# Performance work log

Measured on AMD Instinct MI355X. Metric: run time of the kernel, lower is better.

## Reference

```python
import jax, jax.numpy as jnp
import numpy as np

NV, NH, T, B = 4096, 1024, 64, 32
CDK = 2


def _bern(key, p):
    # torch.bernoulli: sample is non-differentiable
    return jax.lax.stop_gradient((jax.random.uniform(key, p.shape, p.dtype) < p).astype(p.dtype))


def setup_inputs() -> dict:
    key = jax.random.key(0)
    k1, k2, k3 = jax.random.split(key, 3)
    # binary spike-train style visible data [NV, T, B]
    v = (jax.random.uniform(k1, (NV, T, B)) < 0.5).astype(jnp.float32)
    W = 0.01 * jax.random.normal(k2, (NH, NV), jnp.float32)
    U = 0.01 * jax.random.normal(k3, (NH, NH), jnp.float32)
    return {
        "v": v,
        "W": W,
        "U": U,
        "b_v": jnp.zeros((NV,), jnp.float32),
        "b_h": jnp.zeros((NH,), jnp.float32),
        "b_init": jnp.zeros((NH,), jnp.float32),
        "CDk": CDK,
    }


def _cd_step(W, b_v, v_t, hid_bias, key, CDk):
    # hid_bias: [NH,B] = U @ r_lag + b_h[:,None] (or b_init[:,None] at t=0)
    keys = jax.random.split(key, 2 * CDk)
    r_data = jax.nn.sigmoid(W @ v_t + hid_bias)  # hidden means [NH,B]
    h = _bern(keys[0], r_data)
    for k in range(CDk - 1):  # CD-k Gibbs chain (fixed small unroll)
        vm = _bern(keys[2 * k + 1], jax.nn.sigmoid(W.T @ h + b_v[:, None]))
        h = _bern(keys[2 * k + 2], jax.nn.sigmoid(W @ vm + hid_bias))
    v_model = _bern(keys[2 * CDk - 1], jax.nn.sigmoid(W.T @ h + b_v[:, None]))
    return v_model, h, r_data


def reference(v, W, U, b_v, b_h, b_init, CDk):
    Tn = v.shape[1]
    key = jax.random.key(42)
    k0, ks = jax.random.split(key)
    # t = 0 uses b_init instead of U @ r_lag + b_h
    vm0, h0, r0 = _cd_step(W, b_v, v[:, 0, :], b_init[:, None], k0, CDk)
    keys = jax.random.split(ks, Tn - 1)
    v_rest = jnp.moveaxis(v[:, 1:, :], 1, 0)  # [T-1, NV, B]

    def step(r_lag, inp):
        v_t, kt = inp
        vm, h, r = _cd_step(W, b_v, v_t, U @ r_lag + b_h[:, None], kt, CDk)
        return r, (vm, h, r)  # recurrence carries hidden means r_data

    _, (vms, hs, rs) = jax.lax.scan(step, r0, (v_rest, keys))
    v_model = jnp.concatenate([vm0[:, None, :], jnp.moveaxis(vms, 0, 1)], axis=1)  # [NV,T,B]
    r_model = jnp.concatenate([h0[:, None, :], jnp.moveaxis(hs, 0, 1)], axis=1)    # [NH,T,B]
    rt = jnp.concatenate([r0[:, None, :], jnp.moveaxis(rs, 0, 1)], axis=1)         # [NH,T,B]
    return v_model, r_model, rt
```

## Files before the change

### kernel.cpp

```cpp
#include <hip/hip_runtime.h>
#include <cstdint>
#include <cstddef>
#include <math.h>


#define NVV 4096
#define NHH 1024
#define TT  64
#define BB  32
#define CC  2048

typedef int v4i  __attribute__((ext_vector_type(4)));
typedef int v16i __attribute__((ext_vector_type(16)));

__constant__ double SC6[6] = {0x1p-48, 0x1p-40, 0x1p-32, 0x1p-24, 0x1p-16, 0x1p-8};

__host__ __device__ __forceinline__ void tf2x32(uint32_t k0, uint32_t k1,
                                                uint32_t x0, uint32_t x1,
                                                uint32_t& o0, uint32_t& o1) {
  uint32_t ks2 = k0 ^ k1 ^ 0x1BD11BDAu;
#define TF_RND(r) { x0 += x1; x1 = (x1 << (r)) | (x1 >> (32 - (r))); x1 ^= x0; }
  x0 += k0; x1 += k1;
  TF_RND(13) TF_RND(15) TF_RND(26) TF_RND(6)
  x0 += k1;  x1 += ks2 + 1u;
  TF_RND(17) TF_RND(29) TF_RND(16) TF_RND(24)
  x0 += ks2; x1 += k0 + 2u;
  TF_RND(13) TF_RND(15) TF_RND(26) TF_RND(6)
  x0 += k0;  x1 += k1 + 3u;
  TF_RND(17) TF_RND(29) TF_RND(16) TF_RND(24)
  x0 += k1;  x1 += ks2 + 4u;
  TF_RND(13) TF_RND(15) TF_RND(26) TF_RND(6)
  x0 += ks2; x1 += k0 + 5u;
#undef TF_RND
  o0 = x0; o1 = x1;
}

__device__ __forceinline__ float tf_uniform(uint32_t k0, uint32_t k1, uint32_t j) {
  uint32_t o0, o1;
  tf2x32(k0, k1, 0u, j, o0, o1);
  uint32_t bits = o0 ^ o1;
  return __uint_as_float((bits >> 9) | 0x3f800000u) - 1.0f;
}

__device__ __forceinline__ void bern_sample(double logit, uint32_t k0, uint32_t k1,
                                            uint32_t j, float& p32, float& bit) {
  double pd = 1.0 / (1.0 + exp(-logit));
  p32 = (float)pd;
  float u = tf_uniform(k0, k1, j);
  bit = (u < p32) ? 1.0f : 0.0f;
}

__device__ __forceinline__ void step_key(int t, int phase,
                                         uint32_t rk00, uint32_t rk01,
                                         uint32_t rk10, uint32_t rk11,
                                         uint32_t& c0, uint32_t& c1) {
  uint32_t kt0, kt1;
  tf2x32(rk10, rk11, 0u, (uint32_t)(t > 0 ? t - 1 : 0), kt0, kt1);
  if (t == 0) { kt0 = rk00; kt1 = rk01; }
  tf2x32(kt0, kt1, 0u, (uint32_t)phase, c0, c1);
}

__device__ __forceinline__ void slice6(float w, signed char sb[6]) {
  long long v = __double2ll_rn((double)w * 0x1p48);
#pragma unroll
  for (int s = 0; s < 6; s++) {
    signed char b = (signed char)(v & 0xFF);
    sb[s] = b;
    v = (v - b) >> 8;
  }
}

__global__ __launch_bounds__(256)
void prepW(const float* __restrict__ W, signed char* __restrict__ Ws,
           signed char* __restrict__ WsT) {
  __shared__ float tl[64][65];
  int bi = blockIdx.x >> 6;
  int bj = blockIdx.x & 63;
  int n0 = bi * 64, k0 = bj * 64;
  int tid = threadIdx.x;
#pragma unroll
  for (int it = 0; it < 4; it++) {
    int r = (tid >> 4) + it * 16, c4 = (tid & 15) * 4;
    float4 q = *(const float4*)(W + (size_t)(n0 + r) * NVV + k0 + c4);
    tl[r][c4] = q.x; tl[r][c4 + 1] = q.y; tl[r][c4 + 2] = q.z; tl[r][c4 + 3] = q.w;
  }
  __syncthreads();
#pragma unroll
  for (int it = 0; it < 4; it++) {
    int r = (tid >> 4) + it * 16, c4 = (tid & 15) * 4;
    unsigned int pk[6] = {0, 0, 0, 0, 0, 0};
    for (int j = 0; j < 4; j++) {
      signed char sb[6]; slice6(tl[r][c4 + j], sb);
      for (int s = 0; s < 6; s++) pk[s] |= ((unsigned)(unsigned char)sb[s]) << (8 * j);
    }
    for (int s = 0; s < 6; s++)
      *(unsigned int*)(Ws + (size_t)s * NHH * NVV + (size_t)(n0 + r) * NVV + k0 + c4) = pk[s];
  }
#pragma unroll
  for (int it = 0; it < 4; it++) {
    int r = (tid >> 4) + it * 16, c4 = (tid & 15) * 4;
    unsigned int pk[6] = {0, 0, 0, 0, 0, 0};
    for (int j = 0; j < 4; j++) {
      signed char sb[6]; slice6(tl[c4 + j][r], sb);
      for (int s = 0; s < 6; s++) pk[s] |= ((unsigned)(unsigned char)sb[s]) << (8 * j);
    }
    for (int s = 0; s < 6; s++)
      *(unsigned int*)(WsT + (size_t)s * NVV * NHH + (size_t)(k0 + r) * NHH + n0 + c4) = pk[s];
  }
}

__global__ __launch_bounds__(256)
void prepVT(const float* __restrict__ v, signed char* __restrict__ vT) {
  __shared__ float tl[64][65];
  int bi = blockIdx.x >> 5;
  int bj = blockIdx.x & 31;
  int i0 = bi * 64, c0 = bj * 64;
  int tid = threadIdx.x;
#pragma unroll
  for (int it = 0; it < 4; it++) {
    int r = (tid >> 4) + it * 16, c4 = (tid & 15) * 4;
    float4 q = *(const float4*)(v + (size_t)(i0 + r) * CC + c0 + c4);
    tl[r][c4] = q.x; tl[r][c4 + 1] = q.y; tl[r][c4 + 2] = q.z; tl[r][c4 + 3] = q.w;
  }
  __syncthreads();
#pragma unroll
  for (int it = 0; it < 4; it++) {
    int cc = (tid >> 4) + it * 16, i4 = (tid & 15) * 4;
    unsigned int pk = 0;
    for (int j = 0; j < 4; j++)
      pk |= ((unsigned)(tl[i4 + j][cc] != 0.0f ? 1 : 0)) << (8 * j);
    *(unsigned int*)(vT + (size_t)(c0 + cc) * NVV + i0 + i4) = pk;
  }
}

__global__ __launch_bounds__(256)
void s0k(const signed char* __restrict__ vT, const signed char* __restrict__ Ws,
         double* __restrict__ WvT) {
  int wave = threadIdx.x >> 6, lane = threadIdx.x & 63;
  int lrow = lane & 31, lhalf = lane >> 5;
  int xcd = blockIdx.x & 7, idx = blockIdx.x >> 3;
  int bn = xcd * 2 + (idx >> 4);
  int bm = idx & 15;
  int m0 = bm * 128 + (wave & 1) * 64;
  int n0 = bn * 64 + (wave >> 1) * 32;

  v16i acc[2][6];
  for (int mt = 0; mt < 2; mt++)
    for (int s = 0; s < 6; s++)
      for (int e = 0; e < 16; e++) acc[mt][s][e] = 0;

  const signed char* a0 = vT + (size_t)(m0 + lrow) * NVV + 16 * lhalf;
  const signed char* a1 = a0 + (size_t)32 * NVV;
  const signed char* bB = Ws + (size_t)(n0 + lrow) * NVV + 16 * lhalf;
#pragma unroll 2
  for (int kb = 0; kb < NVV; kb += 32) {
    v4i af0 = *(const v4i*)(a0 + kb);
    v4i af1 = *(const v4i*)(a1 + kb);
#pragma unroll
    for (int s = 0; s < 6; s++) {
      v4i bf = *(const v4i*)(bB + (size_t)s * NHH * NVV + kb);
      acc[0][s] = __builtin_amdgcn_mfma_i32_32x32x32_i8(af0, bf, acc[0][s], 0, 0, 0);
      acc[1][s] = __builtin_amdgcn_mfma_i32_32x32x32_i8(af1, bf, acc[1][s], 0, 0, 0);
    }
  }
#pragma unroll
  for (int mt = 0; mt < 2; mt++)
#pragma unroll
    for (int e = 0; e < 16; e++) {
      int row = (e & 3) + 8 * (e >> 2) + 4 * lhalf;
      double lg = 0;
#pragma unroll
      for (int s = 0; s < 6; s++) lg += (double)acc[mt][s][e] * SC6[s];
      WvT[(size_t)(m0 + mt * 32 + row) * NHH + n0 + lrow] = lg;
    }
}

__global__ __launch_bounds__(256)
void step1(const float* __restrict__ U, const float* __restrict__ rin,
           float* __restrict__ rout, const double* __restrict__ WvT,
           const float* __restrict__ b_h, const float* __restrict__ b_init,
           float* __restrict__ rt, unsigned char* __restrict__ hT,
           double* __restrict__ hb64, int t, uint32_t key0, uint32_t key1) {
  __shared__ double red[2][4][32];
  int tid = threadIdx.x;
  int b = tid & 31, ks = (tid >> 5) & 3, rr = tid >> 7;
  int n = blockIdx.x * 2 + rr;
  double a0 = 0, a1 = 0, a2 = 0, a3 = 0;
  if (t > 0) {
    const float* urow = U + (size_t)n * NHH + ks * 256;
    const float* rp = rin + b;
    for (int k = 0; k < 256; k += 4) {
      float4 uq = *(const float4*)(urow + k);
      int kk = (ks * 256 + k) * 32;
      a0 += (double)uq.x * (double)rp[kk];
      a1 += (double)uq.y * (double)rp[kk + 32];
      a2 += (double)uq.z * (double)rp[kk + 64];
      a3 += (double)uq.w * (double)rp[kk + 96];
    }
  }
  red[rr][ks][b] = (a0 + a1) + (a2 + a3);
  __syncthreads();
  if (ks == 0) {
    double s = red[rr][0][b] + red[rr][1][b] + red[rr][2][b] + red[rr][3][b];
    double hbv = (t > 0) ? (s + (double)b_h[n]) : (double)b_init[n];
    double wv = WvT[(size_t)(t * 32 + b) * NHH + n];
    float p32, bit;
    bern_sample(wv + hbv, key0, key1, (uint32_t)(n * 32 + b), p32, bit);
    rt[(size_t)n * CC + t * 32 + b] = p32;
    rout[n * 32 + b] = p32;
    hT[(size_t)(t * 32 + b) * NHH + n] = (unsigned char)(bit != 0.0f ? 1 : 0);
    hb64[(size_t)(t * 32 + b) * NHH + n] = hbv;
  }
}

__global__ __launch_bounds__(256, 2)
void sV(const signed char* __restrict__ WsT, const signed char* __restrict__ xT,
        const float* __restrict__ b_v, unsigned char* __restrict__ bitT,
        float* __restrict__ f32out, int phase,
        uint32_t rk00, uint32_t rk01, uint32_t rk10, uint32_t rk11) {
  int wave = threadIdx.x >> 6, lane = threadIdx.x & 63;
  int lrow = lane & 31, lhalf = lane >> 5;
  int xcd = blockIdx.x & 7, idx = blockIdx.x >> 3;
  int bi = xcd * 8 + (idx & 7);
  int bc = idx >> 3;
  int m0 = bi * 64 + (wave & 1) * 32;
  int n0 = bc * 128 + (wave >> 1) * 64;

  v16i acc[2][6];
  for (int ct = 0; ct < 2; ct++)
    for (int s = 0; s < 6; s++)
      for (int e = 0; e < 16; e++) acc[ct][s][e] = 0;

  const signed char* b0 = xT + (size_t)(n0 + lrow) * NHH + 16 * lhalf;
  const signed char* b1 = b0 + (size_t)32 * NHH;
  const signed char* aB = WsT + (size_t)(m0 + lrow) * NHH + 16 * lhalf;
#pragma unroll 2
  for (int kb = 0; kb < NHH; kb += 32) {
    v4i bf0 = *(const v4i*)(b0 + kb);
    v4i bf1 = *(const v4i*)(b1 + kb);
#pragma unroll
    for (int s = 0; s < 6; s++) {
      v4i af = *(const v4i*)(aB + (size_t)s * NVV * NHH + kb);
      acc[0][s] = __builtin_amdgcn_mfma_i32_32x32x32_i8(af, bf0, acc[0][s], 0, 0, 0);
      acc[1][s] = __builtin_amdgcn_mfma_i32_32x32x32_i8(af, bf1, acc[1][s], 0, 0, 0);
    }
  }

#pragma unroll
  for (int ct = 0; ct < 2; ct++) {
    int tt = (n0 + ct * 32) >> 5;
    uint32_t ck0, ck1;
    step_key(tt, phase, rk00, rk01, rk10, rk11, ck0, ck1);
    int c = n0 + ct * 32 + lrow;
    if (bitT) {
#pragma unroll
      for (int g = 0; g < 4; g++) {
        unsigned int packed = 0;
#pragma unroll
        for (int q = 0; q < 4; q++) {
          int e = g * 4 + q;
          int i = m0 + q + 8 * g + 4 * lhalf;
          double lg = (double)b_v[i];
#pragma unroll
          for (int s = 0; s < 6; s++) lg += (double)acc[ct][s][e] * SC6[s];
          float p32, bit;
          bern_sample(lg, ck0, ck1, (uint32_t)(i * 32 + lrow), p32, bit);
          (void)p32;
          packed |= ((unsigned)(bit != 0.0f ? 1 : 0)) << (8 * q);
        }
        *(unsigned int*)(bitT + (size_t)c * NVV + m0 + 8 * g + 4 * lhalf) = packed;
      }
    } else {
#pragma unroll
      for (int e = 0; e < 16; e++) {
        int i = m0 + (e & 3) + 8 * (e >> 2) + 4 * lhalf;
        double lg = (double)b_v[i];
#pragma unroll
        for (int s = 0; s < 6; s++) lg += (double)acc[ct][s][e] * SC6[s];
        float p32, bit;
        bern_sample(lg, ck0, ck1, (uint32_t)(i * 32 + lrow), p32, bit);
        (void)p32;
        f32out[(size_t)i * CC + c] = bit;
      }
    }
  }
}

__global__ __launch_bounds__(256)
void s3k(const signed char* __restrict__ vmT, const signed char* __restrict__ Ws,
         const double* __restrict__ hb64,
         unsigned char* __restrict__ h2T, float* __restrict__ rmodel,
         uint32_t rk00, uint32_t rk01, uint32_t rk10, uint32_t rk11) {
  int wave = threadIdx.x >> 6, lane = threadIdx.x & 63;
  int lrow = lane & 31, lhalf = lane >> 5;
  int xcd = blockIdx.x & 7, idx = blockIdx.x >> 3;
  int bn = xcd * 2 + (idx >> 4);
  int bm = idx & 15;
  int m0 = bm * 128 + (wave & 1) * 64;
  int n0 = bn * 64 + (wave >> 1) * 32;

  v16i acc[2][6];
  for (int mt = 0; mt < 2; mt++)
    for (int s = 0; s < 6; s++)
      for (int e = 0; e < 16; e++) acc[mt][s][e] = 0;

  const signed char* a0 = vmT + (size_t)(m0 + lrow) * NVV + 16 * lhalf;
  const signed char* a1 = a0 + (size_t)32 * NVV;
  const signed char* bB = Ws + (size_t)(n0 + lrow) * NVV + 16 * lhalf;
#pragma unroll 2
  for (int kb = 0; kb < NVV; kb += 32) {
    v4i af0 = *(const v4i*)(a0 + kb);
    v4i af1 = *(const v4i*)(a1 + kb);
#pragma unroll
    for (int s = 0; s < 6; s++) {
      v4i bf = *(const v4i*)(bB + (size_t)s * NHH * NVV + kb);
      acc[0][s] = __builtin_amdgcn_mfma_i32_32x32x32_i8(af0, bf, acc[0][s], 0, 0, 0);
      acc[1][s] = __builtin_amdgcn_mfma_i32_32x32x32_i8(af1, bf, acc[1][s], 0, 0, 0);
    }
  }

  int n = n0 + lrow;
#pragma unroll
  for (int mt = 0; mt < 2; mt++) {
    int tt = (m0 + mt * 32) >> 5;
    uint32_t ck0, ck1;
    step_key(tt, 2, rk00, rk01, rk10, rk11, ck0, ck1);
#pragma unroll
    for (int e = 0; e < 16; e++) {
      int row = (e & 3) + 8 * (e >> 2) + 4 * lhalf;
      int c = m0 + mt * 32 + row;
      double lg = 0;
#pragma unroll
      for (int s = 0; s < 6; s++) lg += (double)acc[mt][s][e] * SC6[s];
      lg += hb64[(size_t)c * NHH + n];
      float p32, bit;
      bern_sample(lg, ck0, ck1, (uint32_t)(n * 32 + row), p32, bit);
      (void)p32;
      h2T[(size_t)c * NHH + n] = (unsigned char)(bit != 0.0f ? 1 : 0);
      rmodel[(size_t)n * CC + c] = bit;
    }
  }
}

static void tf_split(const uint32_t key[2], int n, uint32_t out[][2]) {
  for (int i = 0; i < n; i++)
    tf2x32(key[0], key[1], 0u, (uint32_t)i, out[i][0], out[i][1]);
}

extern "C" void kernel_launch(void* const* d_in, const int* in_sizes, int n_in,
                              void* d_out, int out_size, void* d_ws, size_t ws_size,
                              hipStream_t stream) {
  const float* v      = (const float*)d_in[0];
  const float* W      = (const float*)d_in[1];
  const float* U      = (const float*)d_in[2];
  const float* b_v    = (const float*)d_in[3];
  const float* b_h    = (const float*)d_in[4];
  const float* b_init = (const float*)d_in[5];

  float* out    = (float*)d_out;
  float* vmodel = out;
  float* rmodel = out + (size_t)NVV * CC;
  float* rt     = rmodel + (size_t)NHH * CC;

  char* wsb = (char*)d_ws;
  signed char* Ws   = (signed char*)wsb;
  signed char* WsT  = (signed char*)(wsb + 25165824);
  signed char* vT   = (signed char*)(wsb + 50331648);
  signed char* vmT  = (signed char*)(wsb + 58720256);
  unsigned char* hT = (unsigned char*)(wsb + 67108864);
  unsigned char* h2T= (unsigned char*)(wsb + 69206016);
  double* WvT       = (double*)(wsb + 71303168);
  double* hb64      = (double*)(wsb + 88080384);
  float* r_cmp      = (float*)(wsb + 104857600);

  uint32_t root[2] = {0u, 42u};
  uint32_t rk[2][2];  tf_split(root, 2, rk);
  uint32_t tk[63][2]; tf_split(rk[1], 63, tk);

  hipLaunchKernelGGL(prepW, dim3(1024), dim3(256), 0, stream, W, Ws, WsT);
  hipLaunchKernelGGL(prepVT, dim3(2048), dim3(256), 0, stream, v, vT);

  hipLaunchKernelGGL(s0k, dim3(256), dim3(256), 0, stream, vT, Ws, WvT);

  for (int t = 0; t < TT; t++) {
    uint32_t key_t0 = t ? tk[t - 1][0] : rk[0][0];
    uint32_t key_t1 = t ? tk[t - 1][1] : rk[0][1];
    uint32_t ck0, ck1;
    tf2x32(key_t0, key_t1, 0u, 0u, ck0, ck1);
    float* rin  = r_cmp + ((t + 1) & 1) * 32768;
    float* rout = r_cmp + (t & 1) * 32768;
    hipLaunchKernelGGL(step1, dim3(512), dim3(256), 0, stream,
                       U, rin, rout, WvT, b_h, b_init, rt, hT, hb64, t, ck0, ck1);
  }

  hipLaunchKernelGGL(sV, dim3(1024), dim3(256), 0, stream,
                     WsT, (const signed char*)hT, b_v, (unsigned char*)vmT,
                     (float*)nullptr, 1, rk[0][0], rk[0][1], rk[1][0], rk[1][1]);

  hipLaunchKernelGGL(s3k, dim3(256), dim3(256), 0, stream,
                     vmT, Ws, hb64, h2T, rmodel,
                     rk[0][0], rk[0][1], rk[1][0], rk[1][1]);

  hipLaunchKernelGGL(sV, dim3(1024), dim3(256), 0, stream,
                     WsT, (const signed char*)h2T, b_v, (unsigned char*)nullptr,
                     vmodel, 3, rk[0][0], rk[0][1], rk[1][0], rk[1][1]);

  (void)in_sizes; (void)n_in; (void)out_size; (void)ws_size;
}
```

Before: 1.346 ms.

## Fuse the per-timestep recurrence into one cooperative kernel and cut weight slices to five

The 64 per-timestep step1 launches become a single cooperative kernel, step1_all, that loops over time with grid.sync() between steps. Each block keeps its four rows of U in shared memory, and the recurrent state is stored batch-major so both operands load as float4. Separately, the int8 weight decomposition drops from six slices to five (scale 2^40 instead of 2^48), which removes one sixth of the MFMA work and weight traffic in every GEMM. The fewer slices lower the fixed-point precision of W and may change sampled bits where a logit sits near a threshold. The grid barriers replace kernel-launch overhead with their own synchronisation cost.

New measurement: 5.361 ms. 298% more time.

```diff
diff --git a/kernel.cpp b/kernel.cpp
--- a/kernel.cpp
+++ b/kernel.cpp
@@ -1,7 +1,10 @@
 #include <hip/hip_runtime.h>
+#include <hip/hip_cooperative_groups.h>
 #include <cstdint>
 #include <cstddef>
 #include <math.h>
+
+namespace cg = cooperative_groups;
 
 
 #define NVV 4096
@@ -9,11 +12,12 @@
 #define TT  64
 #define BB  32
 #define CC  2048
+#define NSL 5
 
 typedef int v4i  __attribute__((ext_vector_type(4)));
 typedef int v16i __attribute__((ext_vector_type(16)));
 
-__constant__ double SC6[6] = {0x1p-48, 0x1p-40, 0x1p-32, 0x1p-24, 0x1p-16, 0x1p-8};
+__constant__ double SC5[NSL] = {0x1p-40, 0x1p-32, 0x1p-24, 0x1p-16, 0x1p-8};
 
 __host__ __device__ __forceinline__ void tf2x32(uint32_t k0, uint32_t k1,
                                                 uint32_t x0, uint32_t x1,
@@ -60,10 +64,10 @@
   tf2x32(kt0, kt1, 0u, (uint32_t)phase, c0, c1);
 }
 
-__device__ __forceinline__ void slice6(float w, signed char sb[6]) {
-  long long v = __double2ll_rn((double)w * 0x1p48);
-#pragma unroll
-  for (int s = 0; s < 6; s++) {
+__device__ __forceinline__ void slice5W(float w, signed char sb[NSL]) {
+  long long v = __double2ll_rn((double)w * 0x1p40);
+#pragma unroll
+  for (int s = 0; s < NSL; s++) {
     signed char b = (signed char)(v & 0xFF);
     sb[s] = b;
     v = (v - b) >> 8;
@@ -88,23 +92,23 @@
 #pragma unroll
   for (int it = 0; it < 4; it++) {
     int r = (tid >> 4) + it * 16, c4 = (tid & 15) * 4;
-    unsigned int pk[6] = {0, 0, 0, 0, 0, 0};
+    unsigned int pk[NSL] = {0, 0, 0, 0, 0};
     for (int j = 0; j < 4; j++) {
-      signed char sb[6]; slice6(tl[r][c4 + j], sb);
-      for (int s = 0; s < 6; s++) pk[s] |= ((unsigned)(unsigned char)sb[s]) << (8 * j);
-    }
-    for (int s = 0; s < 6; s++)
+      signed char sb[NSL]; slice5W(tl[r][c4 + j], sb);
+      for (int s = 0; s < NSL; s++) pk[s] |= ((unsigned)(unsigned char)sb[s]) << (8 * j);
+    }
+    for (int s = 0; s < NSL; s++)
       *(unsigned int*)(Ws + (size_t)s * NHH * NVV + (size_t)(n0 + r) * NVV + k0 + c4) = pk[s];
   }
 #pragma unroll
   for (int it = 0; it < 4; it++) {
     int r = (tid >> 4) + it * 16, c4 = (tid & 15) * 4;
-    unsigned int pk[6] = {0, 0, 0, 0, 0, 0};
+    unsigned int pk[NSL] = {0, 0, 0, 0, 0};
     for (int j = 0; j < 4; j++) {
-      signed char sb[6]; slice6(tl[c4 + j][r], sb);
-      for (int s = 0; s < 6; s++) pk[s] |= ((unsigned)(unsigned char)sb[s]) << (8 * j);
-    }
-    for (int s = 0; s < 6; s++)
+      signed char sb[NSL]; slice5W(tl[c4 + j][r], sb);
+      for (int s = 0; s < NSL; s++) pk[s] |= ((unsigned)(unsigned char)sb[s]) << (8 * j);
+    }
+    for (int s = 0; s < NSL; s++)
       *(unsigned int*)(WsT + (size_t)s * NVV * NHH + (size_t)(k0 + r) * NHH + n0 + c4) = pk[s];
   }
 }
@@ -144,9 +148,9 @@
   int m0 = bm * 128 + (wave & 1) * 64;
   int n0 = bn * 64 + (wave >> 1) * 32;
 
-  v16i acc[2][6];
+  v16i acc[2][NSL];
   for (int mt = 0; mt < 2; mt++)
-    for (int s = 0; s < 6; s++)
+    for (int s = 0; s < NSL; s++)
       for (int e = 0; e < 16; e++) acc[mt][s][e] = 0;
 
   const signed char* a0 = vT + (size_t)(m0 + lrow) * NVV + 16 * lhalf;
@@ -157,7 +161,7 @@
     v4i af0 = *(const v4i*)(a0 + kb);
     v4i af1 = *(const v4i*)(a1 + kb);
 #pragma unroll
-    for (int s = 0; s < 6; s++) {
+    for (int s = 0; s < NSL; s++) {
       v4i bf = *(const v4i*)(bB + (size_t)s * NHH * NVV + kb);
       acc[0][s] = __builtin_amdgcn_mfma_i32_32x32x32_i8(af0, bf, acc[0][s], 0, 0, 0);
       acc[1][s] = __builtin_amdgcn_mfma_i32_32x32x32_i8(af1, bf, acc[1][s], 0, 0, 0);
@@ -170,46 +174,69 @@
       int row = (e & 3) + 8 * (e >> 2) + 4 * lhalf;
       double lg = 0;
 #pragma unroll
-      for (int s = 0; s < 6; s++) lg += (double)acc[mt][s][e] * SC6[s];
+      for (int s = 0; s < NSL; s++) lg += (double)acc[mt][s][e] * SC5[s];
       WvT[(size_t)(m0 + mt * 32 + row) * NHH + n0 + lrow] = lg;
     }
 }
 
 __global__ __launch_bounds__(256)
-void step1(const float* __restrict__ U, const float* __restrict__ rin,
-           float* __restrict__ rout, const double* __restrict__ WvT,
-           const float* __restrict__ b_h, const float* __restrict__ b_init,
-           float* __restrict__ rt, unsigned char* __restrict__ hT,
-           double* __restrict__ hb64, int t, uint32_t key0, uint32_t key1) {
-  __shared__ double red[2][4][32];
+void step1_all(const float* __restrict__ U, const double* __restrict__ WvT,
+               const float* __restrict__ b_h, const float* __restrict__ b_init,
+               float* __restrict__ rt, unsigned char* __restrict__ hT,
+               double* __restrict__ hb64, float* __restrict__ rbuf,
+               uint32_t rk00, uint32_t rk01, uint32_t rk10, uint32_t rk11) {
+  cg::grid_group grid = cg::this_grid();
+  __shared__ float Ush[4 * NHH];
+  __shared__ double red[4][32];
   int tid = threadIdx.x;
-  int b = tid & 31, ks = (tid >> 5) & 3, rr = tid >> 7;
-  int n = blockIdx.x * 2 + rr;
-  double a0 = 0, a1 = 0, a2 = 0, a3 = 0;
-  if (t > 0) {
-    const float* urow = U + (size_t)n * NHH + ks * 256;
-    const float* rp = rin + b;
-    for (int k = 0; k < 256; k += 4) {
-      float4 uq = *(const float4*)(urow + k);
-      int kk = (ks * 256 + k) * 32;
-      a0 += (double)uq.x * (double)rp[kk];
-      a1 += (double)uq.y * (double)rp[kk + 32];
-      a2 += (double)uq.z * (double)rp[kk + 64];
-      a3 += (double)uq.w * (double)rp[kk + 96];
-    }
-  }
-  red[rr][ks][b] = (a0 + a1) + (a2 + a3);
+  int b = tid & 31, ks = (tid >> 5) & 1, rr = tid >> 6;
+  int n = blockIdx.x * 4 + rr;
+
+  {
+    const float4* src = (const float4*)(U + (size_t)blockIdx.x * 4 * NHH);
+    float4* dst = (float4*)Ush;
+    for (int i = tid; i < NHH; i += 256) dst[i] = src[i];
+  }
   __syncthreads();
-  if (ks == 0) {
-    double s = red[rr][0][b] + red[rr][1][b] + red[rr][2][b] + red[rr][3][b];
-    double hbv = (t > 0) ? (s + (double)b_h[n]) : (double)b_init[n];
-    double wv = WvT[(size_t)(t * 32 + b) * NHH + n];
-    float p32, bit;
-    bern_sample(wv + hbv, key0, key1, (uint32_t)(n * 32 + b), p32, bit);
-    rt[(size_t)n * CC + t * 32 + b] = p32;
-    rout[n * 32 + b] = p32;
-    hT[(size_t)(t * 32 + b) * NHH + n] = (unsigned char)(bit != 0.0f ? 1 : 0);
-    hb64[(size_t)(t * 32 + b) * NHH + n] = hbv;
+
+  for (int t = 0; t < TT; t++) {
+    double sum = 0;
+    if (t > 0) {
+      const float* ur = Ush + rr * NHH + ks * 512;
+      const float* rrow = rbuf + ((t + 1) & 1) * (BB * NHH) + b * NHH + ks * 512;
+      double a0 = 0, a1 = 0, a2 = 0, a3 = 0;
+#pragma unroll 4
+      for (int k = 0; k < 512; k += 4) {
+        float4 uq = *(const float4*)(ur + k);
+        float4 rq = *(const float4*)(rrow + k);
+        a0 += (double)uq.x * (double)rq.x;
+        a1 += (double)uq.y * (double)rq.y;
+        a2 += (double)uq.z * (double)rq.z;
+        a3 += (double)uq.w * (double)rq.w;
+      }
+      sum = (a0 + a1) + (a2 + a3);
+    }
+    if (ks == 1) red[rr][b] = sum;
+    __syncthreads();
+    if (ks == 0) {
+      double s = sum + red[rr][b];
+      double hbv = (t > 0) ? (s + (double)b_h[n]) : (double)b_init[n];
+      int c = t * 32 + b;
+      double wv = WvT[(size_t)c * NHH + n];
+      uint32_t kt0, kt1, ck0, ck1;
+      if (t > 0) { tf2x32(rk10, rk11, 0u, (uint32_t)(t - 1), kt0, kt1); }
+      else       { kt0 = rk00; kt1 = rk01; }
+      tf2x32(kt0, kt1, 0u, 0u, ck0, ck1);
+      float p32, bit;
+      bern_sample(wv + hbv, ck0, ck1, (uint32_t)(n * 32 + b), p32, bit);
+      rt[(size_t)n * CC + c] = p32;
+      hT[(size_t)c * NHH + n] = (unsigned char)(bit != 0.0f ? 1 : 0);
+      hb64[(size_t)c * NHH + n] = hbv;
+      rbuf[(t & 1) * (BB * NHH) + b * NHH + n] = p32;
+    }
+    __syncthreads();
+    __threadfence();
+    grid.sync();
   }
 }
 
@@ -226,9 +253,9 @@
   int m0 = bi * 64 + (wave & 1) * 32;
   int n0 = bc * 128 + (wave >> 1) * 64;
 
-  v16i acc[2][6];
+  v16i acc[2][NSL];
   for (int ct = 0; ct < 2; ct++)
-    for (int s = 0; s < 6; s++)
+    for (int s = 0; s < NSL; s++)
       for (int e = 0; e < 16; e++) acc[ct][s][e] = 0;
 
   const signed char* b0 = xT + (size_t)(n0 + lrow) * NHH + 16 * lhalf;
@@ -239,7 +266,7 @@
     v4i bf0 = *(const v4i*)(b0 + kb);
     v4i bf1 = *(const v4i*)(b1 + kb);
 #pragma unroll
-    for (int s = 0; s < 6; s++) {
+    for (int s = 0; s < NSL; s++) {
       v4i af = *(const v4i*)(aB + (size_t)s * NVV * NHH + kb);
       acc[0][s] = __builtin_amdgcn_mfma_i32_32x32x32_i8(af, bf0, acc[0][s], 0, 0, 0);
       acc[1][s] = __builtin_amdgcn_mfma_i32_32x32x32_i8(af, bf1, acc[1][s], 0, 0, 0);
@@ -262,7 +289,7 @@
           int i = m0 + q + 8 * g + 4 * lhalf;
           double lg = (double)b_v[i];
 #pragma unroll
-          for (int s = 0; s < 6; s++) lg += (double)acc[ct][s][e] * SC6[s];
+          for (int s = 0; s < NSL; s++) lg += (double)acc[ct][s][e] * SC5[s];
           float p32, bit;
           bern_sample(lg, ck0, ck1, (uint32_t)(i * 32 + lrow), p32, bit);
           (void)p32;
@@ -276,7 +303,7 @@
         int i = m0 + (e & 3) + 8 * (e >> 2) + 4 * lhalf;
         double lg = (double)b_v[i];
 #pragma unroll
-        for (int s = 0; s < 6; s++) lg += (double)acc[ct][s][e] * SC6[s];
+        for (int s = 0; s < NSL; s++) lg += (double)acc[ct][s][e] * SC5[s];
         float p32, bit;
         bern_sample(lg, ck0, ck1, (uint32_t)(i * 32 + lrow), p32, bit);
         (void)p32;
@@ -299,9 +326,9 @@
   int m0 = bm * 128 + (wave & 1) * 64;
   int n0 = bn * 64 + (wave >> 1) * 32;
 
-  v16i acc[2][6];
+  v16i acc[2][NSL];
   for (int mt = 0; mt < 2; mt++)
-    for (int s = 0; s < 6; s++)
+    for (int s = 0; s < NSL; s++)
       for (int e = 0; e < 16; e++) acc[mt][s][e] = 0;
 
   const signed char* a0 = vmT + (size_t)(m0 + lrow) * NVV + 16 * lhalf;
@@ -312,7 +339,7 @@
     v4i af0 = *(const v4i*)(a0 + kb);
     v4i af1 = *(const v4i*)(a1 + kb);
 #pragma unroll
-    for (int s = 0; s < 6; s++) {
+    for (int s = 0; s < NSL; s++) {
       v4i bf = *(const v4i*)(bB + (size_t)s * NHH * NVV + kb);
       acc[0][s] = __builtin_amdgcn_mfma_i32_32x32x32_i8(af0, bf, acc[0][s], 0, 0, 0);
       acc[1][s] = __builtin_amdgcn_mfma_i32_32x32x32_i8(af1, bf, acc[1][s], 0, 0, 0);
@@ -331,7 +358,7 @@
       int c = m0 + mt * 32 + row;
       double lg = 0;
 #pragma unroll
-      for (int s = 0; s < 6; s++) lg += (double)acc[mt][s][e] * SC6[s];
+      for (int s = 0; s < NSL; s++) lg += (double)acc[mt][s][e] * SC5[s];
       lg += hb64[(size_t)c * NHH + n];
       float p32, bit;
       bern_sample(lg, ck0, ck1, (uint32_t)(n * 32 + row), p32, bit);
@@ -364,33 +391,30 @@
 
   char* wsb = (char*)d_ws;
   signed char* Ws   = (signed char*)wsb;
-  signed char* WsT  = (signed char*)(wsb + 25165824);
-  signed char* vT   = (signed char*)(wsb + 50331648);
-  signed char* vmT  = (signed char*)(wsb + 58720256);
-  unsigned char* hT = (unsigned char*)(wsb + 67108864);
-  unsigned char* h2T= (unsigned char*)(wsb + 69206016);
-  double* WvT       = (double*)(wsb + 71303168);
-  double* hb64      = (double*)(wsb + 88080384);
-  float* r_cmp      = (float*)(wsb + 104857600);
+  signed char* WsT  = (signed char*)(wsb + 20971520);
+  signed char* vT   = (signed char*)(wsb + 41943040);
+  signed char* vmT  = (signed char*)(wsb + 50331648);
+  unsigned char* hT = (unsigned char*)(wsb + 58720256);
+  unsigned char* h2T= (unsigned char*)(wsb + 60817408);
+  double* WvT       = (double*)(wsb + 62914560);
+  double* hb64      = (double*)(wsb + 79691776);
+  float* rbuf       = (float*)(wsb + 96468992);
 
   uint32_t root[2] = {0u, 42u};
   uint32_t rk[2][2];  tf_split(root, 2, rk);
-  uint32_t tk[63][2]; tf_split(rk[1], 63, tk);
 
   hipLaunchKernelGGL(prepW, dim3(1024), dim3(256), 0, stream, W, Ws, WsT);
   hipLaunchKernelGGL(prepVT, dim3(2048), dim3(256), 0, stream, v, vT);
 
   hipLaunchKernelGGL(s0k, dim3(256), dim3(256), 0, stream, vT, Ws, WvT);
 
-  for (int t = 0; t < TT; t++) {
-    uint32_t key_t0 = t ? tk[t - 1][0] : rk[0][0];
-    uint32_t key_t1 = t ? tk[t - 1][1] : rk[0][1];
-    uint32_t ck0, ck1;
-    tf2x32(key_t0, key_t1, 0u, 0u, ck0, ck1);
-    float* rin  = r_cmp + ((t + 1) & 1) * 32768;
-    float* rout = r_cmp + (t & 1) * 32768;
-    hipLaunchKernelGGL(step1, dim3(512), dim3(256), 0, stream,
-                       U, rin, rout, WvT, b_h, b_init, rt, hT, hb64, t, ck0, ck1);
+  {
+    uint32_t k00 = rk[0][0], k01 = rk[0][1], k10 = rk[1][0], k11 = rk[1][1];
+    void* args[] = {(void*)&U, (void*)&WvT, (void*)&b_h, (void*)&b_init,
+                    (void*)&rt, (void*)&hT, (void*)&hb64, (void*)&rbuf,
+                    (void*)&k00, (void*)&k01, (void*)&k10, (void*)&k11};
+    hipLaunchCooperativeKernel((void*)step1_all, dim3(256), dim3(256),
+                               args, 0, stream);
   }
 
   hipLaunchKernelGGL(sV, dim3(1024), dim3(256), 0, stream,
```
